# Optimization experiments

Measured on AMD Instinct MI355X. Metric: run time of the kernel, lower is better.

## Reference

```python
import jax, jax.numpy as jnp
import numpy as np

D_MODEL = 1024
NUM_HEADS = 16
D_K = D_MODEL // NUM_HEADS


def setup_inputs() -> dict:
    key = jax.random.key(0)
    kq, kk, kv, k1, k2, k3, k4 = jax.random.split(key, 7)
    B, S = 2, 2048
    # Xavier-uniform init for square [d_model, d_model] weights
    limit = float(np.sqrt(6.0 / (D_MODEL + D_MODEL)))
    def xav(k):
        return jax.random.uniform(k, (D_MODEL, D_MODEL), jnp.float32, -limit, limit)
    return {
        "query": jax.random.normal(kq, (B, S, D_MODEL), jnp.float32),
        "key": jax.random.normal(kk, (B, S, D_MODEL), jnp.float32),
        "value": jax.random.normal(kv, (B, S, D_MODEL), jnp.float32),
        "W_q": xav(k1),
        "W_k": xav(k2),
        "W_v": xav(k3),
        "W_o": xav(k4),
    }


def reference(query, key, value, W_q, W_k, W_v, W_o):
    B, Sq, _ = query.shape
    Sk = key.shape[1]
    # Linear layers: y = x @ W.T (torch nn.Linear convention)
    Q = (query @ W_q.T).reshape(B, Sq, NUM_HEADS, D_K).transpose(0, 2, 1, 3)
    K = (key @ W_k.T).reshape(B, Sk, NUM_HEADS, D_K).transpose(0, 2, 1, 3)
    V = (value @ W_v.T).reshape(B, Sk, NUM_HEADS, D_K).transpose(0, 2, 1, 3)
    scale = 1.0 / jnp.sqrt(jnp.asarray(D_K, Q.dtype))
    scores = jnp.einsum("bhqd,bhkd->bhqk", Q, K) * scale  # [B,H,Sq,Sk]
    attn = jax.nn.softmax(scores, axis=-1)
    # dropout is identity in eval mode
    out = jnp.einsum("bhqk,bhkd->bhqd", attn, V)
    out = out.transpose(0, 2, 1, 3).reshape(B, Sq, D_MODEL)
    return out @ W_o.T
```

## Files before the change

### kernel.cpp

```cpp
#include <hip/hip_runtime.h>
#include <math.h>

typedef unsigned short ushort_t;
typedef __attribute__((ext_vector_type(8))) short short8;
typedef __attribute__((ext_vector_type(4))) float f32x4;
typedef __attribute__((ext_vector_type(16))) float f32x16;
typedef __attribute__((ext_vector_type(4))) unsigned short ushort4v;
typedef __attribute__((ext_vector_type(2))) unsigned int uint2v;
typedef __attribute__((ext_vector_type(4))) unsigned int uint4v;

#define D_MODEL 1024
#define SEQ 2048
#define MROWS 4096
#define PLANE (MROWS * D_MODEL)
#define WELEM (D_MODEL * D_MODEL)

static __device__ __forceinline__ ushort_t f2bf(float f) {
    unsigned u = __builtin_bit_cast(unsigned, f);
    return (ushort_t)((u + 0x7fffu + ((u >> 16) & 1u)) >> 16);
}
static __device__ __forceinline__ unsigned cvtpk(float lo, float hi) {
    unsigned r;
    asm("v_cvt_pk_bf16_f32 %0, %1, %2" : "=v"(r) : "v"(lo), "v"(hi));
    return r;
}

#define GLDS16(gp, lp)                                                         \
    __builtin_amdgcn_global_load_lds(                                          \
        (const __attribute__((address_space(1))) void*)(gp),                   \
        (__attribute__((address_space(3))) void*)(lp), 16, 0, 0)

__global__ __launch_bounds__(256)
void cvt_all(const float* __restrict__ q, const float* __restrict__ k,
             const float* __restrict__ v, const float* __restrict__ w0,
             const float* __restrict__ w1, const float* __restrict__ w2,
             const float* __restrict__ w3, ushort_t* __restrict__ dst) {
    int blk = blockIdx.x;
    const float* s;
    size_t base;
    if (blk < 6144) {
        const int p = blk >> 11;
        s = (p == 0) ? q : (p == 1) ? k : v;
        base = (size_t)p * PLANE;
        blk &= 2047;
    } else {
        const int p = (blk - 6144) >> 9;
        s = (p == 0) ? w0 : (p == 1) ? w1 : (p == 2) ? w2 : w3;
        base = 3 * (size_t)PLANE + (size_t)p * WELEM;
        blk = (blk - 6144) & 511;
    }
    const int i = (blk * 256 + threadIdx.x) * 8;
    float4 a = *(const float4*)(s + i);
    float4 bb = *(const float4*)(s + i + 4);
    short8 o;
    o[0] = (short)f2bf(a.x); o[1] = (short)f2bf(a.y);
    o[2] = (short)f2bf(a.z); o[3] = (short)f2bf(a.w);
    o[4] = (short)f2bf(bb.x); o[5] = (short)f2bf(bb.y);
    o[6] = (short)f2bf(bb.z); o[7] = (short)f2bf(bb.w);
    *(short8*)(dst + base + i) = o;
}

__global__ __launch_bounds__(256)
void gemm3(const ushort_t* __restrict__ Xq, const ushort_t* __restrict__ Wb,
           ushort_t* __restrict__ Cb) {
    __shared__ __align__(16) ushort_t As[128 * 64];
    __shared__ __align__(16) ushort_t Bs[128 * 64];

    const int z = blockIdx.z;
    const ushort_t* A = Xq + (size_t)z * PLANE;
    const ushort_t* B = Wb + (size_t)z * WELEM;
    ushort_t* C = Cb + (size_t)z * PLANE;

    const int tid = threadIdx.x;
    const int lane = tid & 63;
    const int wid = tid >> 6;
    const int wr = wid >> 1, wc = wid & 1;
    const int brow = blockIdx.y * 128;
    const int bcol = blockIdx.x * 128;

    const int lrow = lane >> 3;
    const int loff = ((lane & 7) ^ lrow) * 8;

    const ushort_t* aS[4];
    const ushort_t* bS[4];
#pragma unroll
    for (int i = 0; i < 4; ++i) {
        aS[i] = A + (size_t)(brow + wid * 32 + i * 8 + lrow) * D_MODEL + loff;
        bS[i] = B + (size_t)(bcol + wid * 32 + i * 8 + lrow) * D_MODEL + loff;
    }

    f32x4 acc[4][4];
#pragma unroll
    for (int i = 0; i < 4; ++i)
#pragma unroll
        for (int j = 0; j < 4; ++j) acc[i][j] = {0.f, 0.f, 0.f, 0.f};

    const int fr = lane & 15, fg = lane >> 4;

    for (int k0 = 0; k0 < D_MODEL; k0 += 64) {
        __syncthreads();
#pragma unroll
        for (int i = 0; i < 4; ++i) {
            GLDS16(aS[i] + k0, As + (wid * 32 + i * 8) * 64);
            GLDS16(bS[i] + k0, Bs + (wid * 32 + i * 8) * 64);
        }
        __syncthreads();
#pragma unroll
        for (int ks = 0; ks < 2; ++ks) {
            const int coff = (ks * 32 + fg * 8) ^ ((fr & 7) << 3);
            short8 af[4], bw[4];
#pragma unroll
            for (int mi = 0; mi < 4; ++mi)
                af[mi] = *(const short8*)&As[(wr * 64 + mi * 16 + fr) * 64 + coff];
#pragma unroll
            for (int nj = 0; nj < 4; ++nj)
                bw[nj] = *(const short8*)&Bs[(wc * 64 + nj * 16 + fr) * 64 + coff];
#pragma unroll
            for (int mi = 0; mi < 4; ++mi)
#pragma unroll
                for (int nj = 0; nj < 4; ++nj)
                    acc[mi][nj] = __builtin_amdgcn_mfma_f32_16x16x32_bf16(
                        af[mi], bw[nj], acc[mi][nj], 0, 0, 0);
        }
    }

    if (z < 2) {
#pragma unroll
        for (int mi = 0; mi < 4; ++mi)
#pragma unroll
            for (int nj = 0; nj < 4; ++nj) {
                const int n = bcol + wc * 64 + nj * 16 + fr;
#pragma unroll
                for (int r = 0; r < 4; ++r) {
                    const int m = brow + wr * 64 + mi * 16 + fg * 4 + r;
                    C[(size_t)m * D_MODEL + n] = f2bf(acc[mi][nj][r]);
                }
            }
    } else {
#pragma unroll
        for (int mi = 0; mi < 4; ++mi)
#pragma unroll
            for (int nj = 0; nj < 4; ++nj) {
                const int n = bcol + wc * 64 + nj * 16 + fr;
                const int m0 = brow + wr * 64 + mi * 16 + fg * 4;
                ushort4v o4;
#pragma unroll
                for (int r = 0; r < 4; ++r) o4[r] = f2bf(acc[mi][nj][r]);
                *(ushort4v*)&C[((size_t)(m0 >> 11) << 21) + (size_t)n * SEQ + (m0 & 2047)] = o4;
            }
    }
}

__global__ __launch_bounds__(256)
void gemm_wo(const ushort_t* __restrict__ A, const ushort_t* __restrict__ B,
             float* __restrict__ C) {
    __shared__ __align__(16) ushort_t As[128 * 64];
    __shared__ __align__(16) ushort_t Bs[128 * 64];

    const int tid = threadIdx.x;
    const int lane = tid & 63;
    const int wid = tid >> 6;
    const int wr = wid >> 1, wc = wid & 1;
    const int brow = blockIdx.y * 128;
    const int bcol = blockIdx.x * 128;

    const int lrow = lane >> 3;
    const int loff = ((lane & 7) ^ lrow) * 8;

    const ushort_t* aS[4];
    const ushort_t* bS[4];
#pragma unroll
    for (int i = 0; i < 4; ++i) {
        aS[i] = A + (size_t)(brow + wid * 32 + i * 8 + lrow) * D_MODEL + loff;
        bS[i] = B + (size_t)(bcol + wid * 32 + i * 8 + lrow) * D_MODEL + loff;
    }

    f32x4 acc[4][4];
#pragma unroll
    for (int i = 0; i < 4; ++i)
#pragma unroll
        for (int j = 0; j < 4; ++j) acc[i][j] = {0.f, 0.f, 0.f, 0.f};

    const int fr = lane & 15, fg = lane >> 4;

    for (int k0 = 0; k0 < D_MODEL; k0 += 64) {
        __syncthreads();
#pragma unroll
        for (int i = 0; i < 4; ++i) {
            GLDS16(aS[i] + k0, As + (wid * 32 + i * 8) * 64);
            GLDS16(bS[i] + k0, Bs + (wid * 32 + i * 8) * 64);
        }
        __syncthreads();
#pragma unroll
        for (int ks = 0; ks < 2; ++ks) {
            const int coff = (ks * 32 + fg * 8) ^ ((fr & 7) << 3);
            short8 af[4], bw[4];
#pragma unroll
            for (int mi = 0; mi < 4; ++mi)
                af[mi] = *(const short8*)&As[(wr * 64 + mi * 16 + fr) * 64 + coff];
#pragma unroll
            for (int nj = 0; nj < 4; ++nj)
                bw[nj] = *(const short8*)&Bs[(wc * 64 + nj * 16 + fr) * 64 + coff];
#pragma unroll
            for (int mi = 0; mi < 4; ++mi)
#pragma unroll
                for (int nj = 0; nj < 4; ++nj)
                    acc[mi][nj] = __builtin_amdgcn_mfma_f32_16x16x32_bf16(
                        af[mi], bw[nj], acc[mi][nj], 0, 0, 0);
        }
    }

#pragma unroll
    for (int mi = 0; mi < 4; ++mi)
#pragma unroll
        for (int nj = 0; nj < 4; ++nj) {
            const int n = bcol + wc * 64 + nj * 16 + fr;
#pragma unroll
            for (int r = 0; r < 4; ++r) {
                const int m = brow + wr * 64 + mi * 16 + fg * 4 + r;
                C[(size_t)m * D_MODEL + n] = acc[mi][nj][r];
            }
        }
}

__global__ __launch_bounds__(512, 4)
void attn_mfma(const ushort_t* __restrict__ Qp, const ushort_t* __restrict__ Kp,
               const ushort_t* __restrict__ VT, ushort_t* __restrict__ Ap) {
    __shared__ __align__(16) ushort_t KVbuf[2][2][4096];
    __shared__ __align__(16) ushort_t Qs[128 * 64];
    __shared__ float sm[2][128];
    __shared__ float sl[2][128];

    const int tid = threadIdx.x;
    const int lane = tid & 63;
    const int wid = tid >> 6;
    const int qgrp = wid & 3;
    const int khalf = wid >> 2;
    const int bid = blockIdx.x;
    const int qt = bid & 15;
    const int h = (bid >> 4) & 15;
    const int b = bid >> 8;

    const int lrow = lane >> 3;
    const int loff = ((lane & 7) ^ lrow) * 8;
    const int q31 = lane & 31;
    const int hi = lane >> 5;

    const int m0 = b * SEQ + qt * 128;

#pragma unroll
    for (int j = 0; j < 2; ++j) {
        const ushort_t* qS =
            Qp + (size_t)(m0 + wid * 16 + j * 8 + lrow) * D_MODEL + h * 64 + loff;
        GLDS16(qS, Qs + (wid * 16 + j * 8) * 64);
    }
    const ushort_t* kS =
        Kp + (size_t)(b * SEQ + wid * 8 + lrow) * D_MODEL + h * 64 + loff;
    const ushort_t* vS =
        VT + ((size_t)b << 21) + (size_t)(h * 64 + wid * 8 + lrow) * SEQ + loff;
    GLDS16(kS, KVbuf[0][0] + wid * 512);
    GLDS16(vS, KVbuf[1][0] + wid * 512);
    kS += 64 * D_MODEL;
    vS += 64;
    __syncthreads();

    const int qrow = qgrp * 32 + q31;
    const int rsw = q31 & 7;
    short8 aq[4];
#pragma unroll
    for (int s = 0; s < 4; ++s)
        aq[s] = *(const short8*)&Qs[qrow * 64 + (((s * 2 + hi) ^ rsw) * 8)];

    f32x16 accO[2];
#pragma unroll
    for (int db = 0; db < 2; ++db)
#pragma unroll
        for (int r = 0; r < 16; ++r) accO[db][r] = 0.f;
    float m_s = -INFINITY;
    float l_p = 0.f;

    const float CEXP = 0.18033688011112042f;
    const int kbase = khalf * 32;

    int cur = 0;
    for (int kt = 0; kt < SEQ / 64; ++kt) {
        __syncthreads();
        if (kt + 1 < SEQ / 64) {
            GLDS16(kS, KVbuf[0][cur ^ 1] + wid * 512);
            GLDS16(vS, KVbuf[1][cur ^ 1] + wid * 512);
            kS += 64 * D_MODEL;
            vS += 64;
        }

        f32x16 accS;
#pragma unroll
        for (int r = 0; r < 16; ++r) accS[r] = 0.f;
        __builtin_amdgcn_s_setprio(1);
#pragma unroll
        for (int s = 0; s < 4; ++s) {
            short8 ak = *(const short8*)&KVbuf[0][cur][(kbase + q31) * 64 +
                                                       (((s * 2 + hi) ^ rsw) * 8)];
            accS = __builtin_amdgcn_mfma_f32_32x32x16_bf16(ak, aq[s], accS, 0, 0, 0);
        }
        __builtin_amdgcn_s_setprio(0);

        float mx = accS[0];
#pragma unroll
        for (int r = 1; r < 16; ++r) mx = fmaxf(mx, accS[r]);
        mx = fmaxf(mx, __shfl_xor(mx, 32));
        const float cand = mx * CEXP;
        if (__any(cand > m_s + 8.f)) {
            const float mnew = fmaxf(m_s, cand);
            const float al = __builtin_amdgcn_exp2f(m_s - mnew);
            m_s = mnew;
            l_p *= al;
#pragma unroll
            for (int db = 0; db < 2; ++db)
#pragma unroll
                for (int r = 0; r < 16; ++r) accO[db][r] *= al;
        }
        float ps = 0.f;
        const float nm = -m_s;
#pragma unroll
        for (int r = 0; r < 16; ++r) {
            const float p = __builtin_amdgcn_exp2f(fmaf(accS[r], CEXP, nm));
            accS[r] = p;
            ps += p;
        }
        l_p += ps;

        short8 pf[2];
#pragma unroll
        for (int ks2 = 0; ks2 < 2; ++ks2) {
            const int bse = ks2 * 8;
            unsigned w0 = cvtpk(accS[bse + 0], accS[bse + 1]);
            unsigned w1 = cvtpk(accS[bse + 2], accS[bse + 3]);
            unsigned w2 = cvtpk(accS[bse + 4], accS[bse + 5]);
            unsigned w3 = cvtpk(accS[bse + 6], accS[bse + 7]);
            asm("v_permlane32_swap_b32 %0, %1" : "+v"(w0), "+v"(w2));
            asm("v_permlane32_swap_b32 %0, %1" : "+v"(w1), "+v"(w3));
            uint4v u = {w0, w1, w2, w3};
            pf[ks2] = __builtin_bit_cast(short8, u);
        }

        __builtin_amdgcn_s_setprio(1);
#pragma unroll
        for (int db = 0; db < 2; ++db)
#pragma unroll
            for (int ks2 = 0; ks2 < 2; ++ks2) {
                short8 av = *(const short8*)&KVbuf[1][cur][(db * 32 + q31) * 64 +
                    (((khalf * 4 + ks2 * 2 + hi) ^ rsw) * 8)];
                accO[db] = __builtin_amdgcn_mfma_f32_32x32x16_bf16(
                    av, pf[ks2], accO[db], 0, 0, 0);
            }
        __builtin_amdgcn_s_setprio(0);
        cur ^= 1;
    }

    const float lt = l_p + __shfl_xor(l_p, 32);
    const int qg = qgrp * 32 + q31;
    if (lane < 32) {
        sm[khalf][qg] = m_s;
        sl[khalf][qg] = lt;
    }
    __syncthreads();
    const float mA = sm[0][qg], mB = sm[1][qg];
    const float mC = fmaxf(mA, mB);
    const float wA = __builtin_amdgcn_exp2f(mA - mC);
    const float wB = __builtin_amdgcn_exp2f(mB - mC);
    const float inv = 1.0f / (wA * sl[0][qg] + wB * sl[1][qg]);

    float* O1 = (float*)KVbuf;
    if (khalf == 1) {
#pragma unroll
        for (int db = 0; db < 2; ++db)
#pragma unroll
            for (int rq = 0; rq < 4; ++rq) {
                f32x4 v;
#pragma unroll
                for (int j = 0; j < 4; ++j) v[j] = accO[db][rq * 4 + j] * wB;
                const int c = db * 8 + rq * 2 + hi;
                *(f32x4*)&O1[qg * 64 + ((c ^ (q31 & 15)) * 4)] = v;
            }
    }
    __syncthreads();
    unsigned* QsW = (unsigned*)Qs;
    if (khalf == 0) {
        const int kkw = 2 * (q31 & 15);
#pragma unroll
        for (int db = 0; db < 2; ++db)
#pragma unroll
            for (int rq = 0; rq < 4; ++rq) {
                const int c = db * 8 + rq * 2 + hi;
                f32x4 o1 = *(const f32x4*)&O1[qg * 64 + ((c ^ (q31 & 15)) * 4)];
                float o0 = (accO[db][rq * 4 + 0] * wA + o1[0]) * inv;
                float o1v = (accO[db][rq * 4 + 1] * wA + o1[1]) * inv;
                float o2 = (accO[db][rq * 4 + 2] * wA + o1[2]) * inv;
                float o3 = (accO[db][rq * 4 + 3] * wA + o1[3]) * inv;
                uint2v u = {cvtpk(o0, o1v), cvtpk(o2, o3)};
                const int c0 = 4 * rq + 2 * hi + 16 * db;
                *(uint2v*)&QsW[qrow * 32 + (c0 ^ kkw)] = u;
            }
    }
    __syncthreads();
#pragma unroll
    for (int pass = 0; pass < 2; ++pass) {
        const int r = wid * 16 + pass * 8 + (lane >> 3);
        const int g8 = lane & 7;
        const int kk = 2 * (r & 15);
        uint2v u0 = *(const uint2v*)&QsW[r * 32 + ((4 * g8) ^ kk)];
        uint2v u1 = *(const uint2v*)&QsW[r * 32 + ((4 * g8 + 2) ^ kk)];
        uint4v o = {u0[0], u0[1], u1[0], u1[1]};
        *(uint4v*)&Ap[(size_t)(m0 + r) * D_MODEL + h * 64 + g8 * 8] = o;
    }
}

extern "C" void kernel_launch(void* const* d_in, const int* in_sizes, int n_in,
                              void* d_out, int out_size, void* d_ws, size_t ws_size,
                              hipStream_t stream) {
    const float* query = (const float*)d_in[0];
    const float* key   = (const float*)d_in[1];
    const float* value = (const float*)d_in[2];
    const float* W_q   = (const float*)d_in[3];
    const float* W_k   = (const float*)d_in[4];
    const float* W_v   = (const float*)d_in[5];
    const float* W_o   = (const float*)d_in[6];
    float* out = (float*)d_out;

    ushort_t* ws = (ushort_t*)d_ws;
    ushort_t* Xq = ws;
    ushort_t* Wb = ws + 3 * (size_t)PLANE;
    ushort_t* Qp = ws + 4 * (size_t)PLANE;
    ushort_t* Kp = Qp + (size_t)PLANE;
    ushort_t* VT = Kp + (size_t)PLANE;
    ushort_t* Ap = VT + (size_t)PLANE;

    cvt_all<<<8192, 256, 0, stream>>>(query, key, value, W_q, W_k, W_v, W_o, Xq);

    dim3 g3(D_MODEL / 128, MROWS / 128, 3);
    gemm3<<<g3, 256, 0, stream>>>(Xq, Wb, Qp);

    attn_mfma<<<512, 512, 0, stream>>>(Qp, Kp, VT, Ap);

    dim3 go(D_MODEL / 128, MROWS / 128);
    gemm_wo<<<go, 256, 0, stream>>>(Ap, Wb + 3 * (size_t)WELEM, out);
}
```

Baseline: 131.8 us.

## Load attention K/V fragments directly to registers and double-buffer output GEMM

The attention kernel stops staging K and V tiles through shared memory. Each wave loads its MFMA fragments straight from global memory, prefetching the next K tile into registers, and the per-iteration block barriers are removed. Block indices are remapped to change scheduling order, and the max/sum reductions use four independent accumulators to shorten dependency chains. The output projection GEMM now uses double-buffered LDS with 128x64 tiles and one barrier per step, at the cost of more global/L2 traffic from the unshared loads.

```diff
diff --git a/kernel.cpp b/kernel.cpp
--- a/kernel.cpp
+++ b/kernel.cpp
@@ -152,69 +152,79 @@
 }
 
 __global__ __launch_bounds__(256)
-void gemm_wo(const ushort_t* __restrict__ A, const ushort_t* __restrict__ B,
-             float* __restrict__ C) {
-    __shared__ __align__(16) ushort_t As[128 * 64];
-    __shared__ __align__(16) ushort_t Bs[128 * 64];
+void gemm_out(const ushort_t* __restrict__ A, const ushort_t* __restrict__ B,
+              float* __restrict__ C) {
+    __shared__ __align__(16) ushort_t As[2][128 * 64];
+    __shared__ __align__(16) ushort_t Bs[2][64 * 64];
 
     const int tid = threadIdx.x;
     const int lane = tid & 63;
     const int wid = tid >> 6;
     const int wr = wid >> 1, wc = wid & 1;
     const int brow = blockIdx.y * 128;
-    const int bcol = blockIdx.x * 128;
+    const int bcol = blockIdx.x * 64;
 
     const int lrow = lane >> 3;
     const int loff = ((lane & 7) ^ lrow) * 8;
 
-    const ushort_t* aS[4];
-    const ushort_t* bS[4];
-#pragma unroll
-    for (int i = 0; i < 4; ++i) {
-        aS[i] = A + (size_t)(brow + wid * 32 + i * 8 + lrow) * D_MODEL + loff;
-        bS[i] = B + (size_t)(bcol + wid * 32 + i * 8 + lrow) * D_MODEL + loff;
-    }
-
-    f32x4 acc[4][4];
+    const ushort_t* aSrc[4];
+    const ushort_t* bSrc[2];
 #pragma unroll
     for (int i = 0; i < 4; ++i)
-#pragma unroll
-        for (int j = 0; j < 4; ++j) acc[i][j] = {0.f, 0.f, 0.f, 0.f};
+        aSrc[i] = A + (size_t)(brow + (wid * 4 + i) * 8 + lrow) * D_MODEL + loff;
+#pragma unroll
+    for (int i = 0; i < 2; ++i)
+        bSrc[i] = B + (size_t)(bcol + (wid * 2 + i) * 8 + lrow) * D_MODEL + loff;
+
+    f32x4 acc[4][2];
+#pragma unroll
+    for (int i = 0; i < 4; ++i)
+#pragma unroll
+        for (int j = 0; j < 2; ++j) acc[i][j] = {0.f, 0.f, 0.f, 0.f};
 
     const int fr = lane & 15, fg = lane >> 4;
 
+#pragma unroll
+    for (int i = 0; i < 4; ++i) GLDS16(aSrc[i], As[0] + (wid * 4 + i) * 512);
+#pragma unroll
+    for (int i = 0; i < 2; ++i) GLDS16(bSrc[i], Bs[0] + (wid * 2 + i) * 512);
+
+    int cur = 0;
     for (int k0 = 0; k0 < D_MODEL; k0 += 64) {
         __syncthreads();
-#pragma unroll
-        for (int i = 0; i < 4; ++i) {
-            GLDS16(aS[i] + k0, As + (wid * 32 + i * 8) * 64);
-            GLDS16(bS[i] + k0, Bs + (wid * 32 + i * 8) * 64);
-        }
-        __syncthreads();
+        if (k0 + 64 < D_MODEL) {
+#pragma unroll
+            for (int i = 0; i < 4; ++i)
+                GLDS16(aSrc[i] + k0 + 64, As[cur ^ 1] + (wid * 4 + i) * 512);
+#pragma unroll
+            for (int i = 0; i < 2; ++i)
+                GLDS16(bSrc[i] + k0 + 64, Bs[cur ^ 1] + (wid * 2 + i) * 512);
+        }
 #pragma unroll
         for (int ks = 0; ks < 2; ++ks) {
             const int coff = (ks * 32 + fg * 8) ^ ((fr & 7) << 3);
-            short8 af[4], bw[4];
+            short8 af[4], bw[2];
 #pragma unroll
             for (int mi = 0; mi < 4; ++mi)
-                af[mi] = *(const short8*)&As[(wr * 64 + mi * 16 + fr) * 64 + coff];
-#pragma unroll
-            for (int nj = 0; nj < 4; ++nj)
-                bw[nj] = *(const short8*)&Bs[(wc * 64 + nj * 16 + fr) * 64 + coff];
+                af[mi] = *(const short8*)&As[cur][(wr * 64 + mi * 16 + fr) * 64 + coff];
+#pragma unroll
+            for (int nj = 0; nj < 2; ++nj)
+                bw[nj] = *(const short8*)&Bs[cur][(wc * 32 + nj * 16 + fr) * 64 + coff];
 #pragma unroll
             for (int mi = 0; mi < 4; ++mi)
 #pragma unroll
-                for (int nj = 0; nj < 4; ++nj)
+                for (int nj = 0; nj < 2; ++nj)
                     acc[mi][nj] = __builtin_amdgcn_mfma_f32_16x16x32_bf16(
                         af[mi], bw[nj], acc[mi][nj], 0, 0, 0);
         }
+        cur ^= 1;
     }
 
 #pragma unroll
     for (int mi = 0; mi < 4; ++mi)
 #pragma unroll
-        for (int nj = 0; nj < 4; ++nj) {
-            const int n = bcol + wc * 64 + nj * 16 + fr;
+        for (int nj = 0; nj < 2; ++nj) {
+            const int n = bcol + wc * 32 + nj * 16 + fr;
 #pragma unroll
             for (int r = 0; r < 4; ++r) {
                 const int m = brow + wr * 64 + mi * 16 + fg * 4 + r;
@@ -226,8 +236,8 @@
 __global__ __launch_bounds__(512, 4)
 void attn_mfma(const ushort_t* __restrict__ Qp, const ushort_t* __restrict__ Kp,
                const ushort_t* __restrict__ VT, ushort_t* __restrict__ Ap) {
-    __shared__ __align__(16) ushort_t KVbuf[2][2][4096];
     __shared__ __align__(16) ushort_t Qs[128 * 64];
+    __shared__ __align__(16) float O1[128 * 64];
     __shared__ float sm[2][128];
     __shared__ float sl[2][128];
 
@@ -236,40 +246,33 @@
     const int wid = tid >> 6;
     const int qgrp = wid & 3;
     const int khalf = wid >> 2;
-    const int bid = blockIdx.x;
+
+    const int bid0 = blockIdx.x;
+    const int bid = (bid0 & 7) * 64 + (bid0 >> 3);
     const int qt = bid & 15;
     const int h = (bid >> 4) & 15;
     const int b = bid >> 8;
 
-    const int lrow = lane >> 3;
-    const int loff = ((lane & 7) ^ lrow) * 8;
     const int q31 = lane & 31;
     const int hi = lane >> 5;
 
     const int m0 = b * SEQ + qt * 128;
 
-#pragma unroll
-    for (int j = 0; j < 2; ++j) {
-        const ushort_t* qS =
-            Qp + (size_t)(m0 + wid * 16 + j * 8 + lrow) * D_MODEL + h * 64 + loff;
-        GLDS16(qS, Qs + (wid * 16 + j * 8) * 64);
-    }
-    const ushort_t* kS =
-        Kp + (size_t)(b * SEQ + wid * 8 + lrow) * D_MODEL + h * 64 + loff;
-    const ushort_t* vS =
-        VT + ((size_t)b << 21) + (size_t)(h * 64 + wid * 8 + lrow) * SEQ + loff;
-    GLDS16(kS, KVbuf[0][0] + wid * 512);
-    GLDS16(vS, KVbuf[1][0] + wid * 512);
-    kS += 64 * D_MODEL;
-    vS += 64;
-    __syncthreads();
-
-    const int qrow = qgrp * 32 + q31;
-    const int rsw = q31 & 7;
+    const ushort_t* qB =
+        Qp + (size_t)(m0 + qgrp * 32 + q31) * D_MODEL + h * 64 + hi * 8;
+    const ushort_t* kB =
+        Kp + (size_t)(b * SEQ + khalf * 32 + q31) * D_MODEL + h * 64 + hi * 8;
+    const ushort_t* vB =
+        VT + ((size_t)b << 21) + (size_t)(h * 64 + q31) * SEQ + khalf * 32 + hi * 8;
+
     short8 aq[4];
 #pragma unroll
-    for (int s = 0; s < 4; ++s)
-        aq[s] = *(const short8*)&Qs[qrow * 64 + (((s * 2 + hi) ^ rsw) * 8)];
+    for (int s = 0; s < 4; ++s) aq[s] = *(const short8*)(qB + s * 16);
+
+    short8 kf[4];
+#pragma unroll
+    for (int s = 0; s < 4; ++s) kf[s] = *(const short8*)(kB + s * 16);
+    kB += 64 * D_MODEL;
 
     f32x16 accO[2];
 #pragma unroll
@@ -280,33 +283,40 @@
     float l_p = 0.f;
 
     const float CEXP = 0.18033688011112042f;
-    const int kbase = khalf * 32;
-
-    int cur = 0;
+
     for (int kt = 0; kt < SEQ / 64; ++kt) {
-        __syncthreads();
-        if (kt + 1 < SEQ / 64) {
-            GLDS16(kS, KVbuf[0][cur ^ 1] + wid * 512);
-            GLDS16(vS, KVbuf[1][cur ^ 1] + wid * 512);
-            kS += 64 * D_MODEL;
-            vS += 64;
-        }
+        short8 vf0[2], vf1[2];
+#pragma unroll
+        for (int ks2 = 0; ks2 < 2; ++ks2) {
+            vf0[ks2] = *(const short8*)(vB + ks2 * 16);
+            vf1[ks2] = *(const short8*)(vB + 32 * SEQ + ks2 * 16);
+        }
+        vB += 64;
 
         f32x16 accS;
 #pragma unroll
         for (int r = 0; r < 16; ++r) accS[r] = 0.f;
         __builtin_amdgcn_s_setprio(1);
 #pragma unroll
-        for (int s = 0; s < 4; ++s) {
-            short8 ak = *(const short8*)&KVbuf[0][cur][(kbase + q31) * 64 +
-                                                       (((s * 2 + hi) ^ rsw) * 8)];
-            accS = __builtin_amdgcn_mfma_f32_32x32x16_bf16(ak, aq[s], accS, 0, 0, 0);
-        }
+        for (int s = 0; s < 4; ++s)
+            accS = __builtin_amdgcn_mfma_f32_32x32x16_bf16(kf[s], aq[s], accS, 0, 0, 0);
         __builtin_amdgcn_s_setprio(0);
 
-        float mx = accS[0];
-#pragma unroll
-        for (int r = 1; r < 16; ++r) mx = fmaxf(mx, accS[r]);
+        if (kt + 1 < SEQ / 64) {
+#pragma unroll
+            for (int s = 0; s < 4; ++s) kf[s] = *(const short8*)(kB + s * 16);
+            kB += 64 * D_MODEL;
+        }
+
+        float ma = accS[0], mb = accS[1], mc = accS[2], md = accS[3];
+#pragma unroll
+        for (int r = 4; r < 16; r += 4) {
+            ma = fmaxf(ma, accS[r + 0]);
+            mb = fmaxf(mb, accS[r + 1]);
+            mc = fmaxf(mc, accS[r + 2]);
+            md = fmaxf(md, accS[r + 3]);
+        }
+        float mx = fmaxf(fmaxf(ma, mb), fmaxf(mc, md));
         mx = fmaxf(mx, __shfl_xor(mx, 32));
         const float cand = mx * CEXP;
         if (__any(cand > m_s + 8.f)) {
@@ -319,15 +329,18 @@
 #pragma unroll
                 for (int r = 0; r < 16; ++r) accO[db][r] *= al;
         }
-        float ps = 0.f;
         const float nm = -m_s;
-#pragma unroll
-        for (int r = 0; r < 16; ++r) {
-            const float p = __builtin_amdgcn_exp2f(fmaf(accS[r], CEXP, nm));
-            accS[r] = p;
-            ps += p;
-        }
-        l_p += ps;
+        float pa = 0.f, pb = 0.f, pc = 0.f, pd = 0.f;
+#pragma unroll
+        for (int r = 0; r < 16; r += 4) {
+            const float p0 = __builtin_amdgcn_exp2f(fmaf(accS[r + 0], CEXP, nm));
+            const float p1 = __builtin_amdgcn_exp2f(fmaf(accS[r + 1], CEXP, nm));
+            const float p2 = __builtin_amdgcn_exp2f(fmaf(accS[r + 2], CEXP, nm));
+            const float p3 = __builtin_amdgcn_exp2f(fmaf(accS[r + 3], CEXP, nm));
+            accS[r + 0] = p0; accS[r + 1] = p1; accS[r + 2] = p2; accS[r + 3] = p3;
+            pa += p0; pb += p1; pc += p2; pd += p3;
+        }
+        l_p += (pa + pb) + (pc + pd);
 
         short8 pf[2];
 #pragma unroll
@@ -345,16 +358,13 @@
 
         __builtin_amdgcn_s_setprio(1);
 #pragma unroll
-        for (int db = 0; db < 2; ++db)
-#pragma unroll
-            for (int ks2 = 0; ks2 < 2; ++ks2) {
-                short8 av = *(const short8*)&KVbuf[1][cur][(db * 32 + q31) * 64 +
-                    (((khalf * 4 + ks2 * 2 + hi) ^ rsw) * 8)];
-                accO[db] = __builtin_amdgcn_mfma_f32_32x32x16_bf16(
-                    av, pf[ks2], accO[db], 0, 0, 0);
-            }
+        for (int ks2 = 0; ks2 < 2; ++ks2) {
+            accO[0] = __builtin_amdgcn_mfma_f32_32x32x16_bf16(vf0[ks2], pf[ks2],
+                                                              accO[0], 0, 0, 0);
+            accO[1] = __builtin_amdgcn_mfma_f32_32x32x16_bf16(vf1[ks2], pf[ks2],
+                                                              accO[1], 0, 0, 0);
+        }
         __builtin_amdgcn_s_setprio(0);
-        cur ^= 1;
     }
 
     const float lt = l_p + __shfl_xor(l_p, 32);
@@ -370,7 +380,6 @@
     const float wB = __builtin_amdgcn_exp2f(mB - mC);
     const float inv = 1.0f / (wA * sl[0][qg] + wB * sl[1][qg]);
 
-    float* O1 = (float*)KVbuf;
     if (khalf == 1) {
 #pragma unroll
         for (int db = 0; db < 2; ++db)
@@ -385,6 +394,7 @@
     }
     __syncthreads();
     unsigned* QsW = (unsigned*)Qs;
+    const int qrow = qgrp * 32 + q31;
     if (khalf == 0) {
         const int kkw = 2 * (q31 & 15);
 #pragma unroll
@@ -442,6 +452,6 @@
 
     attn_mfma<<<512, 512, 0, stream>>>(Qp, Kp, VT, Ap);
 
-    dim3 go(D_MODEL / 128, MROWS / 128);
-    gemm_wo<<<go, 256, 0, stream>>>(Ap, Wb + 3 * (size_t)WELEM, out);
-}
+    dim3 go(D_MODEL / 64, MROWS / 128);
+    gemm_out<<<go, 256, 0, stream>>>(Ap, Wb + 3 * (size_t)WELEM, out);
+}
```

Result: slower. 198.8 us (+50.9%).

## Remap block indices for XCD locality and double-buffer output projection GEMM

Applied to the files above, without the earlier changes.

Block IDs in the QKV GEMM, the attention kernel and the output GEMM are remapped so that consecutive blocks landing on the same XCD (bid mod 8) cover neighbouring tiles, which should improve L2 reuse. The output projection GEMM now uses 128x64 tiles, doubling the grid to 512 blocks to fill more CUs. It also double-buffers its LDS tiles so the next K-slice loads while the current one is computed, with one barrier per iteration. The cost is more LDS per block and a smaller N tile, which lowers arithmetic intensity per block.

```diff
diff --git a/kernel.cpp b/kernel.cpp
--- a/kernel.cpp
+++ b/kernel.cpp
@@ -66,7 +66,13 @@
     __shared__ __align__(16) ushort_t As[128 * 64];
     __shared__ __align__(16) ushort_t Bs[128 * 64];
 
-    const int z = blockIdx.z;
+    const int lin = blockIdx.x + blockIdx.y * 8 + blockIdx.z * 256;
+    const int lin2 = (lin & 7) * 96 + (lin >> 3);
+    const int z = lin2 >> 8;
+    const int rem = lin2 & 255;
+    const int by = rem >> 3;
+    const int bx = rem & 7;
+
     const ushort_t* A = Xq + (size_t)z * PLANE;
     const ushort_t* B = Wb + (size_t)z * WELEM;
     ushort_t* C = Cb + (size_t)z * PLANE;
@@ -75,8 +81,8 @@
     const int lane = tid & 63;
     const int wid = tid >> 6;
     const int wr = wid >> 1, wc = wid & 1;
-    const int brow = blockIdx.y * 128;
-    const int bcol = blockIdx.x * 128;
+    const int brow = by * 128;
+    const int bcol = bx * 128;
 
     const int lrow = lane >> 3;
     const int loff = ((lane & 7) ^ lrow) * 8;
@@ -152,69 +158,84 @@
 }
 
 __global__ __launch_bounds__(256)
-void gemm_wo(const ushort_t* __restrict__ A, const ushort_t* __restrict__ B,
-             float* __restrict__ C) {
-    __shared__ __align__(16) ushort_t As[128 * 64];
-    __shared__ __align__(16) ushort_t Bs[128 * 64];
+void gemm_out(const ushort_t* __restrict__ A, const ushort_t* __restrict__ B,
+              float* __restrict__ C) {
+    __shared__ __align__(16) ushort_t As[2][128 * 64];
+    __shared__ __align__(16) ushort_t Bs[2][64 * 64];
+
+    const int lin = blockIdx.x + blockIdx.y * 16;
+    const int lin2 = (lin & 7) * 64 + (lin >> 3);
+    const int by = lin2 >> 4;
+    const int bx = lin2 & 15;
 
     const int tid = threadIdx.x;
     const int lane = tid & 63;
     const int wid = tid >> 6;
     const int wr = wid >> 1, wc = wid & 1;
-    const int brow = blockIdx.y * 128;
-    const int bcol = blockIdx.x * 128;
+    const int brow = by * 128;
+    const int bcol = bx * 64;
 
     const int lrow = lane >> 3;
     const int loff = ((lane & 7) ^ lrow) * 8;
 
-    const ushort_t* aS[4];
-    const ushort_t* bS[4];
-#pragma unroll
-    for (int i = 0; i < 4; ++i) {
-        aS[i] = A + (size_t)(brow + wid * 32 + i * 8 + lrow) * D_MODEL + loff;
-        bS[i] = B + (size_t)(bcol + wid * 32 + i * 8 + lrow) * D_MODEL + loff;
-    }
-
-    f32x4 acc[4][4];
+    const ushort_t* aSrc[4];
+    const ushort_t* bSrc[2];
 #pragma unroll
     for (int i = 0; i < 4; ++i)
-#pragma unroll
-        for (int j = 0; j < 4; ++j) acc[i][j] = {0.f, 0.f, 0.f, 0.f};
+        aSrc[i] = A + (size_t)(brow + (wid * 4 + i) * 8 + lrow) * D_MODEL + loff;
+#pragma unroll
+    for (int i = 0; i < 2; ++i)
+        bSrc[i] = B + (size_t)(bcol + (wid * 2 + i) * 8 + lrow) * D_MODEL + loff;
+
+    f32x4 acc[4][2];
+#pragma unroll
+    for (int i = 0; i < 4; ++i)
+#pragma unroll
+        for (int j = 0; j < 2; ++j) acc[i][j] = {0.f, 0.f, 0.f, 0.f};
 
     const int fr = lane & 15, fg = lane >> 4;
 
+#pragma unroll
+    for (int i = 0; i < 4; ++i) GLDS16(aSrc[i], As[0] + (wid * 4 + i) * 512);
+#pragma unroll
+    for (int i = 0; i < 2; ++i) GLDS16(bSrc[i], Bs[0] + (wid * 2 + i) * 512);
+
+    int cur = 0;
     for (int k0 = 0; k0 < D_MODEL; k0 += 64) {
         __syncthreads();
-#pragma unroll
-        for (int i = 0; i < 4; ++i) {
-            GLDS16(aS[i] + k0, As + (wid * 32 + i * 8) * 64);
-            GLDS16(bS[i] + k0, Bs + (wid * 32 + i * 8) * 64);
-        }
-        __syncthreads();
+        if (k0 + 64 < D_MODEL) {
+#pragma unroll
+            for (int i = 0; i < 4; ++i)
+                GLDS16(aSrc[i] + k0 + 64, As[cur ^ 1] + (wid * 4 + i) * 512);
+#pragma unroll
+            for (int i = 0; i < 2; ++i)
+                GLDS16(bSrc[i] + k0 + 64, Bs[cur ^ 1] + (wid * 2 + i) * 512);
+        }
 #pragma unroll
         for (int ks = 0; ks < 2; ++ks) {
             const int coff = (ks * 32 + fg * 8) ^ ((fr & 7) << 3);
-            short8 af[4], bw[4];
+            short8 af[4], bw[2];
 #pragma unroll
             for (int mi = 0; mi < 4; ++mi)
-                af[mi] = *(const short8*)&As[(wr * 64 + mi * 16 + fr) * 64 + coff];
-#pragma unroll
-            for (int nj = 0; nj < 4; ++nj)
-                bw[nj] = *(const short8*)&Bs[(wc * 64 + nj * 16 + fr) * 64 + coff];
+                af[mi] = *(const short8*)&As[cur][(wr * 64 + mi * 16 + fr) * 64 + coff];
+#pragma unroll
+            for (int nj = 0; nj < 2; ++nj)
+                bw[nj] = *(const short8*)&Bs[cur][(wc * 32 + nj * 16 + fr) * 64 + coff];
 #pragma unroll
             for (int mi = 0; mi < 4; ++mi)
 #pragma unroll
-                for (int nj = 0; nj < 4; ++nj)
+                for (int nj = 0; nj < 2; ++nj)
                     acc[mi][nj] = __builtin_amdgcn_mfma_f32_16x16x32_bf16(
                         af[mi], bw[nj], acc[mi][nj], 0, 0, 0);
         }
+        cur ^= 1;
     }
 
 #pragma unroll
     for (int mi = 0; mi < 4; ++mi)
 #pragma unroll
-        for (int nj = 0; nj < 4; ++nj) {
-            const int n = bcol + wc * 64 + nj * 16 + fr;
+        for (int nj = 0; nj < 2; ++nj) {
+            const int n = bcol + wc * 32 + nj * 16 + fr;
 #pragma unroll
             for (int r = 0; r < 4; ++r) {
                 const int m = brow + wr * 64 + mi * 16 + fg * 4 + r;
@@ -236,7 +257,9 @@
     const int wid = tid >> 6;
     const int qgrp = wid & 3;
     const int khalf = wid >> 2;
-    const int bid = blockIdx.x;
+
+    const int bid0 = blockIdx.x;
+    const int bid = (bid0 & 7) * 64 + (bid0 >> 3);
     const int qt = bid & 15;
     const int h = (bid >> 4) & 15;
     const int b = bid >> 8;
@@ -442,6 +465,6 @@
 
     attn_mfma<<<512, 512, 0, stream>>>(Qp, Kp, VT, Ap);
 
-    dim3 go(D_MODEL / 128, MROWS / 128);
-    gemm_wo<<<go, 256, 0, stream>>>(Ap, Wb + 3 * (size_t)WELEM, out);
-}
+    dim3 go(D_MODEL / 64, MROWS / 128);
+    gemm_out<<<go, 256, 0, stream>>>(Ap, Wb + 3 * (size_t)WELEM, out);
+}
```

After: 122.7 us. 1.07x faster.
